# Optimization experiments

Measured on AMD Instinct MI355X. Metric: run time of the kernel, lower is better.

The kernel has to match this reference:

```python
import jax, jax.numpy as jnp
import numpy as np

DIM = 2048
DIM_HEAD = 64
NUM_HEADS = 32
FFN_INNER = 4 * DIM  # 8192
ATTN_INNER = NUM_HEADS * DIM_HEAD  # 2048
IN_WIDTH = FFN_INNER * 2 + 3 * ATTN_INNER  # 22528
OUT_IN = FFN_INNER + DIM  # 10240
B, S = 1, 2048


def setup_inputs() -> dict:
    key = jax.random.key(0)
    k0, k1, k2 = jax.random.split(key, 3)
    x = jax.random.normal(k0, (B, S, DIM), dtype=jnp.float32)
    W_in = jax.random.normal(k1, (DIM, IN_WIDTH), dtype=jnp.float32) * (DIM ** -0.5)
    W_out = jax.random.normal(k2, (OUT_IN, DIM), dtype=jnp.float32) * (OUT_IN ** -0.5)
    ln_w = jnp.ones((DIM,), dtype=jnp.float32)
    ln_b = jnp.zeros((DIM,), dtype=jnp.float32)
    return {"x": x, "ln_w": ln_w, "ln_b": ln_b, "W_in": W_in, "W_out": W_out}


def _layernorm(x, w, b, eps=1e-5):
    mu = jnp.mean(x, axis=-1, keepdims=True)
    var = jnp.mean(jnp.square(x - mu), axis=-1, keepdims=True)
    return (x - mu) * jax.lax.rsqrt(var + eps) * w + b


def reference(x, ln_w, ln_b, W_in, W_out):
    b, s, _ = x.shape
    h = _layernorm(x, ln_w, ln_b)
    res = h @ W_in  # [b, s, IN_WIDTH]
    q = res[..., :ATTN_INNER]
    k = res[..., ATTN_INNER:2 * ATTN_INNER]
    v = res[..., 2 * ATTN_INNER:3 * ATTN_INNER]
    ffn_input = res[..., 3 * ATTN_INNER:3 * ATTN_INNER + FFN_INNER]
    # b s (h d) -> b h s d
    q = q.reshape(b, s, NUM_HEADS, DIM_HEAD).transpose(0, 2, 1, 3)
    k = k.reshape(b, s, NUM_HEADS, DIM_HEAD).transpose(0, 2, 1, 3)
    v = v.reshape(b, s, NUM_HEADS, DIM_HEAD).transpose(0, 2, 1, 3)
    q = q * (DIM_HEAD ** -0.5)
    sim = jnp.einsum('bhsd,bhnd->bhsn', q, k)  # [b, h, s, s]
    causal = jnp.triu(jnp.ones((s, s), dtype=bool), k=1)
    sim = jnp.where(causal, -jnp.finfo(sim.dtype).max, sim)
    attn = jax.nn.softmax(sim, axis=-1)
    attn_out = jnp.einsum('bhsn,bhnd->bhsd', attn, v)
    attn_out = attn_out.transpose(0, 2, 1, 3).reshape(b, s, ATTN_INNER)
    concat_input = jnp.concatenate([attn_out, ffn_input], axis=-1)  # [b, s, OUT_IN]
    return concat_input @ W_out
```

## Files before the change

kernel.cpp:

```cpp
#include <hip/hip_runtime.h>
#include <stdint.h>

typedef __bf16 bf16x8 __attribute__((ext_vector_type(8)));
typedef float f32x4 __attribute__((ext_vector_type(4)));
typedef uint16_t u16x4 __attribute__((ext_vector_type(4)));
typedef uint16_t u16x8 __attribute__((ext_vector_type(8)));

#define LOG2E 1.4426950408889634f

__device__ __forceinline__ uint16_t f2bf(float f) {
  union { float f; uint32_t u; } v; v.f = f;
  return (uint16_t)((v.u + 0x7fffu + ((v.u >> 16) & 1u)) >> 16);
}

__device__ __forceinline__ void gload_lds16(const void* g, void* l) {
  __builtin_amdgcn_global_load_lds(
      (const __attribute__((address_space(1))) void*)g,
      (__attribute__((address_space(3))) void*)l, 16, 0, 0);
}

__device__ __forceinline__ f32x4 mfma16(bf16x8 a, bf16x8 b, f32x4 c) {
  return __builtin_amdgcn_mfma_f32_16x16x32_bf16(a, b, c, 0, 0, 0);
}

__global__ __launch_bounds__(256) void ln_kernel(const float* __restrict__ x,
                                                 const float* __restrict__ g,
                                                 const float* __restrict__ bta,
                                                 uint16_t* __restrict__ h) {
  const int row = blockIdx.x;
  const int t = threadIdx.x;
  const float* xr = x + (size_t)row * 2048 + t * 8;
  float4 v0 = *(const float4*)xr;
  float4 v1 = *(const float4*)(xr + 4);
  float s = v0.x + v0.y + v0.z + v0.w + v1.x + v1.y + v1.z + v1.w;
  float q = v0.x*v0.x + v0.y*v0.y + v0.z*v0.z + v0.w*v0.w
          + v1.x*v1.x + v1.y*v1.y + v1.z*v1.z + v1.w*v1.w;
  #pragma unroll
  for (int m = 1; m < 64; m <<= 1) {
    s += __shfl_xor(s, m);
    q += __shfl_xor(q, m);
  }
  __shared__ float ps[4], pq[4];
  const int wid = t >> 6, lane = t & 63;
  if (lane == 0) { ps[wid] = s; pq[wid] = q; }
  __syncthreads();
  s = ps[0] + ps[1] + ps[2] + ps[3];
  q = pq[0] + pq[1] + pq[2] + pq[3];
  const float mu = s * (1.0f / 2048.0f);
  const float var = q * (1.0f / 2048.0f) - mu * mu;
  const float rs = rsqrtf(var + 1e-5f);
  float4 w0 = *(const float4*)(g + t * 8);
  float4 w1 = *(const float4*)(g + t * 8 + 4);
  float4 b0 = *(const float4*)(bta + t * 8);
  float4 b1 = *(const float4*)(bta + t * 8 + 4);
  u16x8 o;
  o[0] = f2bf((v0.x - mu) * rs * w0.x + b0.x);
  o[1] = f2bf((v0.y - mu) * rs * w0.y + b0.y);
  o[2] = f2bf((v0.z - mu) * rs * w0.z + b0.z);
  o[3] = f2bf((v0.w - mu) * rs * w0.w + b0.w);
  o[4] = f2bf((v1.x - mu) * rs * w1.x + b1.x);
  o[5] = f2bf((v1.y - mu) * rs * w1.y + b1.y);
  o[6] = f2bf((v1.z - mu) * rs * w1.z + b1.z);
  o[7] = f2bf((v1.w - mu) * rs * w1.w + b1.w);
  *(u16x8*)(h + (size_t)row * 2048 + t * 8) = o;
}

__global__ __launch_bounds__(256) void transpose_w(const float* __restrict__ in,
                                                   uint16_t* __restrict__ out,
                                                   int R, int ldin,
                                                   int scale_cols, float scale) {
  __shared__ uint16_t tile[64][65];
  const int c0 = blockIdx.x * 64;
  const int r0 = blockIdx.y * 64;
  const int t = threadIdx.x;
  const int cc = (t & 15) * 4;
  const int rb = t >> 4;
  #pragma unroll
  for (int p = 0; p < 4; ++p) {
    const int r = rb + p * 16;
    const float4 v = *(const float4*)(in + (size_t)(r0 + r) * ldin + c0 + cc);
    const float m0 = (c0 + cc + 0) < scale_cols ? scale : 1.0f;
    const float m1 = (c0 + cc + 1) < scale_cols ? scale : 1.0f;
    const float m2 = (c0 + cc + 2) < scale_cols ? scale : 1.0f;
    const float m3 = (c0 + cc + 3) < scale_cols ? scale : 1.0f;
    tile[r][cc + 0] = f2bf(v.x * m0);
    tile[r][cc + 1] = f2bf(v.y * m1);
    tile[r][cc + 2] = f2bf(v.z * m2);
    tile[r][cc + 3] = f2bf(v.w * m3);
  }
  __syncthreads();
  #pragma unroll
  for (int p = 0; p < 4; ++p) {
    const int oc = rb + p * 16;
    u16x4 ov;
    ov.x = tile[cc + 0][oc];
    ov.y = tile[cc + 1][oc];
    ov.z = tile[cc + 2][oc];
    ov.w = tile[cc + 3][oc];
    *(u16x4*)(out + (size_t)(c0 + oc) * R + r0 + cc) = ov;
  }
}

__global__ __launch_bounds__(256) void transpose_v(const uint16_t* __restrict__ res,
                                                   uint16_t* __restrict__ vt) {
  __shared__ uint16_t tile[64][65];
  const int c0 = blockIdx.x * 64;
  const int r0 = blockIdx.y * 64;
  const int t = threadIdx.x;
  const int cc = (t & 15) * 4;
  const int rb = t >> 4;
  #pragma unroll
  for (int p = 0; p < 4; ++p) {
    const int r = rb + p * 16;
    const u16x4 v = *(const u16x4*)(res + (size_t)(r0 + r) * 14336 + 4096 + c0 + cc);
    tile[r][cc + 0] = v.x;
    tile[r][cc + 1] = v.y;
    tile[r][cc + 2] = v.z;
    tile[r][cc + 3] = v.w;
  }
  __syncthreads();
  #pragma unroll
  for (int p = 0; p < 4; ++p) {
    const int oc = rb + p * 16;
    u16x4 ov;
    ov.x = tile[cc + 0][oc];
    ov.y = tile[cc + 1][oc];
    ov.z = tile[cc + 2][oc];
    ov.w = tile[cc + 3][oc];
    *(u16x4*)(vt + (size_t)(c0 + oc) * 2048 + r0 + cc) = ov;
  }
}

template <int CONCAT, int CF32>
__global__ __launch_bounds__(512, 2) void gemm_8p(
    const uint16_t* __restrict__ A0, const uint16_t* __restrict__ A1,
    const uint16_t* __restrict__ B, void* __restrict__ C0, void* __restrict__ C1,
    int ldbK, int ldc, int kchunk, int nt) {
  __shared__ __attribute__((aligned(16))) uint16_t Alds[2 * 256 * 64];
  __shared__ __attribute__((aligned(16))) uint16_t Blds[2 * 256 * 64];
  const int bid = blockIdx.x;
  const int qx = gridDim.x >> 3;
  const int wg = (bid & 7) * qx + (bid >> 3);
  const int m0 = (wg & 7) << 8;
  const int n0 = (wg >> 3) << 8;
  const int sk = blockIdx.y;
  const int k0 = sk * kchunk;
  const int t = threadIdx.x, wid = t >> 6, lane = t & 63;
  const int wr = wid >> 2, wc = wid & 3;

  f32x4 acc[8][4] = {};

  auto stageA = [&](int tt, int h) {
    const int kg = k0 + tt * 64;
    const uint16_t* As; int lda, kc;
    if (CONCAT && kg >= 2048) { As = A1; lda = 14336; kc = kg + 4096; }
    else                      { As = A0; lda = 2048;  kc = kg; }
    char* base = (char*)Alds + (tt & 1) * 32768 + h * 16384;
    #pragma unroll
    for (int j = 0; j < 2; ++j) {
      const int chunk = j * 512 + t;
      const int r = chunk >> 3, s = chunk & 7;
      gload_lds16(As + (size_t)(m0 + h * 128 + r) * lda + kc + ((s ^ (r & 7)) << 3),
                  base + chunk * 16);
    }
  };
  auto stageB = [&](int tt, int h) {
    const int kg = k0 + tt * 64;
    char* base = (char*)Blds + (tt & 1) * 32768 + h * 16384;
    #pragma unroll
    for (int j = 0; j < 2; ++j) {
      const int chunk = j * 512 + t;
      const int r = chunk >> 3, s = chunk & 7;
      gload_lds16(B + (size_t)(n0 + h * 128 + r) * ldbK + kg + ((s ^ (r & 7)) << 3),
                  base + chunk * 16);
    }
  };

  stageB(0, 0); stageB(0, 1); stageA(0, 0); stageA(0, 1);
  stageB(1, 0); stageB(1, 1);
  asm volatile("s_waitcnt vmcnt(4)" ::: "memory");
  __builtin_amdgcn_s_barrier();
  __builtin_amdgcn_sched_barrier(0);

  bf16x8 bf[4][2];
  for (int tt = 0; tt < nt; ++tt) {
    const char* Ab = (const char*)Alds + (tt & 1) * 32768;
    const char* Bb = (const char*)Blds + (tt & 1) * 32768;
    #pragma unroll
    for (int q = 0; q < 4; ++q) {
      if (q == 0) {
        if (tt + 1 < nt) { asm volatile("s_waitcnt vmcnt(4)" ::: "memory"); }
        else             { asm volatile("s_waitcnt vmcnt(0)" ::: "memory"); }
        if (tt + 1 < nt) stageA(tt + 1, 0);
        __builtin_amdgcn_s_barrier();
        __builtin_amdgcn_sched_barrier(0);
        #pragma unroll
        for (int n = 0; n < 4; ++n)
          #pragma unroll
          for (int ks = 0; ks < 2; ++ks) {
            const int r = wc * 64 + n * 16 + (lane & 15);
            const int c = (ks * 4 + (lane >> 4)) ^ (r & 7);
            bf[n][ks] = *(const bf16x8*)(Bb + r * 128 + c * 16);
          }
      } else {
        if (q == 1)      { if (tt + 1 < nt) stageA(tt + 1, 1); }
        else if (q == 2) { if (tt + 2 < nt) stageB(tt + 2, 0); }
        else             { if (tt + 2 < nt) stageB(tt + 2, 1); }
        __builtin_amdgcn_s_barrier();
      }
      bf16x8 af[2][2];
      #pragma unroll
      for (int i = 0; i < 2; ++i)
        #pragma unroll
        for (int ks = 0; ks < 2; ++ks) {
          const int r = wr * 128 + (2 * q + i) * 16 + (lane & 15);
          const int c = (ks * 4 + (lane >> 4)) ^ (r & 7);
          af[i][ks] = *(const bf16x8*)(Ab + r * 128 + c * 16);
        }
      __builtin_amdgcn_s_setprio(1);
      #pragma unroll
      for (int i = 0; i < 2; ++i)
        #pragma unroll
        for (int n = 0; n < 4; ++n) {
          acc[2 * q + i][n] = mfma16(af[i][0], bf[n][0], acc[2 * q + i][n]);
          acc[2 * q + i][n] = mfma16(af[i][1], bf[n][1], acc[2 * q + i][n]);
        }
      __builtin_amdgcn_s_setprio(0);
      __builtin_amdgcn_s_barrier();
    }
  }

  #pragma unroll
  for (int m = 0; m < 8; ++m)
    #pragma unroll
    for (int n = 0; n < 4; ++n)
      #pragma unroll
      for (int r = 0; r < 4; ++r) {
        const int row = m0 + wr * 128 + m * 16 + (lane >> 4) * 4 + r;
        const int col = n0 + wc * 64 + n * 16 + (lane & 15);
        if (CF32) {
          float* C = (sk == 0) ? (float*)C0
                               : ((float*)C1 + (size_t)(sk - 1) * 4194304ull);
          C[(size_t)row * ldc + col] = acc[m][n][r];
        } else {
          ((uint16_t*)C0)[(size_t)row * ldc + col] = f2bf(acc[m][n][r]);
        }
      }
}

__global__ __launch_bounds__(256) void reduce_add3(float* __restrict__ out,
                                                   const float* __restrict__ p) {
  const size_t i = ((size_t)blockIdx.x * 256 + threadIdx.x) * 4;
  float4 a = *(const float4*)(out + i);
  const float4 b = *(const float4*)(p + i);
  const float4 c = *(const float4*)(p + 4194304 + i);
  const float4 d = *(const float4*)(p + 8388608 + i);
  a.x += b.x + c.x + d.x;
  a.y += b.y + c.y + d.y;
  a.z += b.z + c.z + d.z;
  a.w += b.w + c.w + d.w;
  *(float4*)(out + i) = a;
}

__global__ __launch_bounds__(256) void attn_kernel(const uint16_t* __restrict__ res,
                                                   const uint16_t* __restrict__ vt,
                                                   uint16_t* __restrict__ aout) {
  const int qt = blockIdx.x;
  const int hh = blockIdx.y;
  const int q0 = qt * 128;
  const int t = threadIdx.x, wid = t >> 6, lane = t & 63;
  const int qw = q0 + wid * 32;
  __shared__ uint16_t Klds[64 * 64];
  __shared__ uint16_t Vlds[64 * 64];
  __shared__ uint16_t Plds[4 * 32 * 64];
  char* pbase = (char*)Plds + wid * 4096;

  bf16x8 qf[2][2];
  #pragma unroll
  for (int m = 0; m < 2; ++m)
    #pragma unroll
    for (int ks = 0; ks < 2; ++ks)
      qf[m][ks] = *(const bf16x8*)(res + (size_t)(qw + m * 16 + (lane & 15)) * 14336
                                   + hh * 64 + ks * 32 + (lane >> 4) * 8);
  f32x4 O[2][4] = {};
  f32x4 mrun[2], lrun[2];
  #pragma unroll
  for (int m = 0; m < 2; ++m)
    #pragma unroll
    for (int r = 0; r < 4; ++r) { mrun[m][r] = -1e30f; lrun[m][r] = 0.0f; }

  const int nkt = qt * 2 + 2;
  for (int kt = 0; kt < nkt; ++kt) {
    const int k0 = kt * 64;
    __syncthreads();
    #pragma unroll
    for (int i = 0; i < 2; ++i) {
      const int o = (wid * 2 + i) * 1024 + lane * 16;
      const int row = o >> 7;
      const int slot = (o >> 4) & 7;
      const int col = (slot ^ (row & 7)) << 3;
      gload_lds16(res + (size_t)(k0 + row) * 14336 + 2048 + hh * 64 + col,
                  (char*)Klds + (wid * 2 + i) * 1024);
      gload_lds16(vt + (size_t)(hh * 64 + row) * 2048 + k0 + col,
                  (char*)Vlds + (wid * 2 + i) * 1024);
    }
    __syncthreads();
    if (k0 <= qw + 31) {
      f32x4 s[2][4] = {};
      #pragma unroll
      for (int ks = 0; ks < 2; ++ks) {
        bf16x8 kf[4];
        #pragma unroll
        for (int n = 0; n < 4; ++n) {
          const int row = n * 16 + (lane & 15);
          const int slot = (ks * 4 + (lane >> 4)) ^ (row & 7);
          kf[n] = *(const bf16x8*)((const char*)Klds + row * 128 + slot * 16);
        }
        #pragma unroll
        for (int m = 0; m < 2; ++m)
          #pragma unroll
          for (int n = 0; n < 4; ++n)
            s[m][n] = mfma16(qf[m][ks], kf[n], s[m][n]);
      }
      if (k0 + 63 > qw) {
        #pragma unroll
        for (int m = 0; m < 2; ++m)
          #pragma unroll
          for (int n = 0; n < 4; ++n)
            #pragma unroll
            for (int r = 0; r < 4; ++r) {
              const int key = k0 + n * 16 + (lane & 15);
              const int qr = qw + m * 16 + (lane >> 4) * 4 + r;
              if (key > qr) s[m][n][r] = -1e30f;
            }
      }
      #pragma unroll
      for (int m = 0; m < 2; ++m) {
        f32x4 tmax = s[m][0];
        #pragma unroll
        for (int n = 1; n < 4; ++n)
          #pragma unroll
          for (int r = 0; r < 4; ++r) tmax[r] = fmaxf(tmax[r], s[m][n][r]);
        #pragma unroll
        for (int msk = 1; msk < 16; msk <<= 1)
          #pragma unroll
          for (int r = 0; r < 4; ++r) tmax[r] = fmaxf(tmax[r], __shfl_xor(tmax[r], msk));
        f32x4 newm, sc;
        #pragma unroll
        for (int r = 0; r < 4; ++r) {
          newm[r] = fmaxf(mrun[m][r], tmax[r]);
          sc[r] = exp2f((mrun[m][r] - newm[r]) * LOG2E);
          mrun[m][r] = newm[r];
        }
        f32x4 psum;
        #pragma unroll
        for (int r = 0; r < 4; ++r) psum[r] = 0.0f;
        #pragma unroll
        for (int n = 0; n < 4; ++n)
          #pragma unroll
          for (int r = 0; r < 4; ++r) {
            const float p = exp2f((s[m][n][r] - newm[r]) * LOG2E);
            s[m][n][r] = p;
            psum[r] += p;
          }
        #pragma unroll
        for (int msk = 1; msk < 16; msk <<= 1)
          #pragma unroll
          for (int r = 0; r < 4; ++r) psum[r] += __shfl_xor(psum[r], msk);
        #pragma unroll
        for (int r = 0; r < 4; ++r) lrun[m][r] = lrun[m][r] * sc[r] + psum[r];
        #pragma unroll
        for (int d = 0; d < 4; ++d)
          #pragma unroll
          for (int r = 0; r < 4; ++r) O[m][d][r] *= sc[r];
        #pragma unroll
        for (int n = 0; n < 4; ++n)
          #pragma unroll
          for (int r = 0; r < 4; ++r) {
            const int prow = m * 16 + (lane >> 4) * 4 + r;
            const int pcol = n * 16 + (lane & 15);
            *(uint16_t*)(pbase + prow * 128 + (((pcol >> 3) ^ (prow & 7)) << 4)
                         + (pcol & 7) * 2) = f2bf(s[m][n][r]);
          }
      }
      asm volatile("s_waitcnt lgkmcnt(0)" ::: "memory");
      #pragma unroll
      for (int ks = 0; ks < 2; ++ks) {
        bf16x8 pa[2], vf[4];
        #pragma unroll
        for (int m = 0; m < 2; ++m) {
          const int row = m * 16 + (lane & 15);
          const int slot = (ks * 4 + (lane >> 4)) ^ (row & 7);
          pa[m] = *(const bf16x8*)(pbase + row * 128 + slot * 16);
        }
        #pragma unroll
        for (int d = 0; d < 4; ++d) {
          const int row = d * 16 + (lane & 15);
          const int slot = (ks * 4 + (lane >> 4)) ^ (row & 7);
          vf[d] = *(const bf16x8*)((const char*)Vlds + row * 128 + slot * 16);
        }
        #pragma unroll
        for (int m = 0; m < 2; ++m)
          #pragma unroll
          for (int d = 0; d < 4; ++d)
            O[m][d] = mfma16(pa[m], vf[d], O[m][d]);
      }
    }
  }
  #pragma unroll
  for (int m = 0; m < 2; ++m) {
    f32x4 inv;
    #pragma unroll
    for (int r = 0; r < 4; ++r) inv[r] = 1.0f / lrun[m][r];
    #pragma unroll
    for (int d = 0; d < 4; ++d)
      #pragma unroll
      for (int r = 0; r < 4; ++r) {
        const int row = qw + m * 16 + (lane >> 4) * 4 + r;
        const int col = hh * 64 + d * 16 + (lane & 15);
        aout[(size_t)row * 2048 + col] = f2bf(O[m][d][r] * inv[r]);
      }
  }
}

extern "C" void kernel_launch(void* const* d_in, const int* in_sizes, int n_in,
                              void* d_out, int out_size, void* d_ws, size_t ws_size,
                              hipStream_t stream) {
  (void)in_sizes; (void)n_in; (void)out_size;
  const float* x     = (const float*)d_in[0];
  const float* ln_w  = (const float*)d_in[1];
  const float* ln_b  = (const float*)d_in[2];
  const float* W_in  = (const float*)d_in[3];
  const float* W_out = (const float*)d_in[4];

  const size_t need = 184549376ull;
  if (ws_size < need) return;
  char* ws = (char*)d_ws;
  size_t off = 0;
  uint16_t* h     = (uint16_t*)(ws + off); off += (size_t)2048 * 2048 * 2;
  uint16_t* WtIn  = (uint16_t*)(ws + off); off += (size_t)14336 * 2048 * 2;
  uint16_t* WtOut = (uint16_t*)(ws + off); off += (size_t)2048 * 10240 * 2;
  uint16_t* res   = (uint16_t*)(ws + off); off += (size_t)2048 * 14336 * 2;
  uint16_t* vt    = (uint16_t*)(ws + off); off += (size_t)2048 * 2048 * 2;
  uint16_t* aout  = (uint16_t*)(ws + off);
  float* partials = (float*)ws;

  ln_kernel<<<2048, 256, 0, stream>>>(x, ln_w, ln_b, h);
  transpose_w<<<dim3(224, 32), 256, 0, stream>>>(W_in, WtIn, 2048, 22528, 2048, 0.125f);
  transpose_w<<<dim3(32, 160), 256, 0, stream>>>(W_out, WtOut, 10240, 2048, 0, 1.0f);
  gemm_8p<0, 0><<<dim3(448, 1), 512, 0, stream>>>(h, nullptr, WtIn, res, nullptr,
                                                  2048, 14336, 0, 32);
  transpose_v<<<dim3(32, 32), 256, 0, stream>>>(res, vt);
  attn_kernel<<<dim3(16, 32), 256, 0, stream>>>(res, vt, aout);
  gemm_8p<1, 1><<<dim3(64, 4), 512, 0, stream>>>(aout, res, WtOut, d_out, partials,
                                                 10240, 2048, 2560, 40);
  reduce_add3<<<4096, 256, 0, stream>>>((float*)d_out, partials);
}
```

Baseline: 477.9 us.

## Restructure GEMM main loop with register double-buffered A fragments

The GEMM inner loop is rescheduled so A fragments for the next quarter are read from LDS into alternate registers while the current quarter's MFMAs run. The next tile's first A fragment and B fragments are prefetched across the iteration boundary. Global-to-LDS staging now issues the whole next-next tile at once at the end of each iteration instead of spreading it over four quarters. This cuts from four barriers per iteration to two and hides LDS read latency. The cost is more live registers and a full vmcnt(0) wait mid-iteration.

New measurement: 453.8 us. -5.1%, faster.

```diff
diff --git a/kernel.cpp b/kernel.cpp
--- a/kernel.cpp
+++ b/kernel.cpp
@@ -132,7 +132,7 @@
 }
 
 template <int CONCAT, int CF32>
-__global__ __launch_bounds__(512, 2) void gemm_8p(
+__global__ __launch_bounds__(512, 2) void gemm_rp(
     const uint16_t* __restrict__ A0, const uint16_t* __restrict__ A1,
     const uint16_t* __restrict__ B, void* __restrict__ C0, void* __restrict__ C1,
     int ldbK, int ldc, int kchunk, int nt) {
@@ -149,85 +149,84 @@
   const int wr = wid >> 2, wc = wid & 3;
 
   f32x4 acc[8][4] = {};
-
-  auto stageA = [&](int tt, int h) {
+  bf16x8 bf[4][2];
+  bf16x8 afa[2][2], afb[2][2];
+
+  auto stage = [&](int tt) {
     const int kg = k0 + tt * 64;
     const uint16_t* As; int lda, kc;
     if (CONCAT && kg >= 2048) { As = A1; lda = 14336; kc = kg + 4096; }
     else                      { As = A0; lda = 2048;  kc = kg; }
-    char* base = (char*)Alds + (tt & 1) * 32768 + h * 16384;
-    #pragma unroll
-    for (int j = 0; j < 2; ++j) {
+    char* abase = (char*)Alds + (tt & 1) * 32768;
+    char* bbase = (char*)Blds + (tt & 1) * 32768;
+    #pragma unroll
+    for (int j = 0; j < 4; ++j) {
       const int chunk = j * 512 + t;
       const int r = chunk >> 3, s = chunk & 7;
-      gload_lds16(As + (size_t)(m0 + h * 128 + r) * lda + kc + ((s ^ (r & 7)) << 3),
-                  base + chunk * 16);
+      const int col = (s ^ (r & 7)) << 3;
+      gload_lds16(As + (size_t)(m0 + r) * lda + kc + col, abase + chunk * 16);
+      gload_lds16(B + (size_t)(n0 + r) * ldbK + kg + col, bbase + chunk * 16);
     }
   };
-  auto stageB = [&](int tt, int h) {
-    const int kg = k0 + tt * 64;
-    char* base = (char*)Blds + (tt & 1) * 32768 + h * 16384;
-    #pragma unroll
-    for (int j = 0; j < 2; ++j) {
-      const int chunk = j * 512 + t;
-      const int r = chunk >> 3, s = chunk & 7;
-      gload_lds16(B + (size_t)(n0 + h * 128 + r) * ldbK + kg + ((s ^ (r & 7)) << 3),
-                  base + chunk * 16);
-    }
+
+  auto ldA = [&](int buf, int q, bf16x8 af[2][2]) {
+    const char* Ab = (const char*)Alds + buf * 32768;
+    #pragma unroll
+    for (int i = 0; i < 2; ++i)
+      #pragma unroll
+      for (int ks = 0; ks < 2; ++ks) {
+        const int r = wr * 128 + (2 * q + i) * 16 + (lane & 15);
+        const int c = (ks * 4 + (lane >> 4)) ^ (r & 7);
+        af[i][ks] = *(const bf16x8*)(Ab + r * 128 + c * 16);
+      }
   };
-
-  stageB(0, 0); stageB(0, 1); stageA(0, 0); stageA(0, 1);
-  stageB(1, 0); stageB(1, 1);
-  asm volatile("s_waitcnt vmcnt(4)" ::: "memory");
+  auto ldB = [&](int buf) {
+    const char* Bb = (const char*)Blds + buf * 32768;
+    #pragma unroll
+    for (int n = 0; n < 4; ++n)
+      #pragma unroll
+      for (int ks = 0; ks < 2; ++ks) {
+        const int r = wc * 64 + n * 16 + (lane & 15);
+        const int c = (ks * 4 + (lane >> 4)) ^ (r & 7);
+        bf[n][ks] = *(const bf16x8*)(Bb + r * 128 + c * 16);
+      }
+  };
+  auto MF = [&](int q, bf16x8 af[2][2]) {
+    __builtin_amdgcn_s_setprio(1);
+    #pragma unroll
+    for (int i = 0; i < 2; ++i)
+      #pragma unroll
+      for (int n = 0; n < 4; ++n) {
+        acc[2 * q + i][n] = mfma16(af[i][0], bf[n][0], acc[2 * q + i][n]);
+        acc[2 * q + i][n] = mfma16(af[i][1], bf[n][1], acc[2 * q + i][n]);
+      }
+    __builtin_amdgcn_s_setprio(0);
+  };
+
+  stage(0); stage(1);
+  asm volatile("s_waitcnt vmcnt(8)" ::: "memory");
   __builtin_amdgcn_s_barrier();
   __builtin_amdgcn_sched_barrier(0);
-
-  bf16x8 bf[4][2];
+  ldB(0);
+  ldA(0, 0, afa);
+
   for (int tt = 0; tt < nt; ++tt) {
-    const char* Ab = (const char*)Alds + (tt & 1) * 32768;
-    const char* Bb = (const char*)Blds + (tt & 1) * 32768;
-    #pragma unroll
-    for (int q = 0; q < 4; ++q) {
-      if (q == 0) {
-        if (tt + 1 < nt) { asm volatile("s_waitcnt vmcnt(4)" ::: "memory"); }
-        else             { asm volatile("s_waitcnt vmcnt(0)" ::: "memory"); }
-        if (tt + 1 < nt) stageA(tt + 1, 0);
-        __builtin_amdgcn_s_barrier();
-        __builtin_amdgcn_sched_barrier(0);
-        #pragma unroll
-        for (int n = 0; n < 4; ++n)
-          #pragma unroll
-          for (int ks = 0; ks < 2; ++ks) {
-            const int r = wc * 64 + n * 16 + (lane & 15);
-            const int c = (ks * 4 + (lane >> 4)) ^ (r & 7);
-            bf[n][ks] = *(const bf16x8*)(Bb + r * 128 + c * 16);
-          }
-      } else {
-        if (q == 1)      { if (tt + 1 < nt) stageA(tt + 1, 1); }
-        else if (q == 2) { if (tt + 2 < nt) stageB(tt + 2, 0); }
-        else             { if (tt + 2 < nt) stageB(tt + 2, 1); }
-        __builtin_amdgcn_s_barrier();
-      }
-      bf16x8 af[2][2];
-      #pragma unroll
-      for (int i = 0; i < 2; ++i)
-        #pragma unroll
-        for (int ks = 0; ks < 2; ++ks) {
-          const int r = wr * 128 + (2 * q + i) * 16 + (lane & 15);
-          const int c = (ks * 4 + (lane >> 4)) ^ (r & 7);
-          af[i][ks] = *(const bf16x8*)(Ab + r * 128 + c * 16);
-        }
-      __builtin_amdgcn_s_setprio(1);
-      #pragma unroll
-      for (int i = 0; i < 2; ++i)
-        #pragma unroll
-        for (int n = 0; n < 4; ++n) {
-          acc[2 * q + i][n] = mfma16(af[i][0], bf[n][0], acc[2 * q + i][n]);
-          acc[2 * q + i][n] = mfma16(af[i][1], bf[n][1], acc[2 * q + i][n]);
-        }
-      __builtin_amdgcn_s_setprio(0);
-      __builtin_amdgcn_s_barrier();
-    }
+    const int buf = tt & 1, nbuf = buf ^ 1;
+    ldA(buf, 1, afb);
+    MF(0, afa);
+    ldA(buf, 2, afa);
+    MF(1, afb);
+    asm volatile("s_waitcnt vmcnt(0)" ::: "memory");
+    __builtin_amdgcn_s_barrier();
+    __builtin_amdgcn_sched_barrier(0);
+    ldA(buf, 3, afb);
+    MF(2, afa);
+    if (tt + 1 < nt) ldA(nbuf, 0, afa);
+    MF(3, afb);
+    __builtin_amdgcn_s_barrier();
+    __builtin_amdgcn_sched_barrier(0);
+    if (tt + 1 < nt) ldB(nbuf);
+    if (tt + 2 < nt) stage(tt + 2);
   }
 
   #pragma unroll
@@ -448,11 +447,11 @@
   ln_kernel<<<2048, 256, 0, stream>>>(x, ln_w, ln_b, h);
   transpose_w<<<dim3(224, 32), 256, 0, stream>>>(W_in, WtIn, 2048, 22528, 2048, 0.125f);
   transpose_w<<<dim3(32, 160), 256, 0, stream>>>(W_out, WtOut, 10240, 2048, 0, 1.0f);
-  gemm_8p<0, 0><<<dim3(448, 1), 512, 0, stream>>>(h, nullptr, WtIn, res, nullptr,
+  gemm_rp<0, 0><<<dim3(448, 1), 512, 0, stream>>>(h, nullptr, WtIn, res, nullptr,
                                                   2048, 14336, 0, 32);
   transpose_v<<<dim3(32, 32), 256, 0, stream>>>(res, vt);
   attn_kernel<<<dim3(16, 32), 256, 0, stream>>>(res, vt, aout);
-  gemm_8p<1, 1><<<dim3(64, 4), 512, 0, stream>>>(aout, res, WtOut, d_out, partials,
+  gemm_rp<1, 1><<<dim3(64, 4), 512, 0, stream>>>(aout, res, WtOut, d_out, partials,
                                                  10240, 2048, 2560, 40);
   reduce_add3<<<4096, 256, 0, stream>>>((float*)d_out, partials);
 }
```
